# Kernel tuning notes

Hardware: AMD Instinct MI355X
Metric: run time of the kernel (lower is better)

The kernel has to match this reference:

```python
import jax, jax.numpy as jnp
import numpy as np

HEADS = 8
CONTEXT_FRAMES = 128
REL_POS_MAX = 128


def setup_inputs() -> dict:
    key = jax.random.key(0)
    ks = jax.random.split(key, 6)
    b, c, f, t = 2, 512, 64, 512
    x = jax.random.normal(ks[0], (b, c, f, t), dtype=jnp.float32)
    # Linear weights stored as [in, out] (equivalent to torch weight.T)
    W_qkv = jax.random.normal(ks[1], (c, 3 * c), dtype=jnp.float32) * (c ** -0.5)
    b_qkv = jnp.zeros((3 * c,), dtype=jnp.float32)
    W_proj = jax.random.normal(ks[2], (c, c), dtype=jnp.float32) * (c ** -0.5)
    b_proj = jnp.zeros((c,), dtype=jnp.float32)
    rel_pos_bias = jax.random.normal(ks[3], (HEADS, REL_POS_MAX), dtype=jnp.float32) * 0.02
    return {"x": x, "W_qkv": W_qkv, "b_qkv": b_qkv, "W_proj": W_proj,
            "b_proj": b_proj, "rel_pos_bias": rel_pos_bias}


def reference(x, W_qkv, b_qkv, W_proj, b_proj, rel_pos_bias):
    b, c, f, t = x.shape
    hd = c // HEADS
    # (b, c, f, t) -> (b*f, t, c)
    h = jnp.transpose(x, (0, 2, 3, 1)).reshape(b * f, t, c)
    qkv = (h @ W_qkv + b_qkv).reshape(b * f, t, 3, HEADS, hd)
    q, k, v = qkv[:, :, 0], qkv[:, :, 1], qkv[:, :, 2]  # [bf, t, H, hd]
    scale = hd ** -0.5
    scores = jnp.einsum('nqhd,nkhd->nhqk', q, k) * scale  # [bf, H, t, t]
    # causal band mask + gathered relative-position bias
    dist = jnp.arange(t)[:, None] - jnp.arange(t)[None, :]  # [t, t]
    invalid = (dist < 0) | (dist >= CONTEXT_FRAMES)
    bias = rel_pos_bias[:, jnp.clip(dist, 0, REL_POS_MAX - 1)]  # [H, t, t]
    scores = scores + bias[None]
    scores = jnp.where(invalid[None, None], -jnp.inf, scores)
    attn = jax.nn.softmax(scores, axis=-1)
    y = jnp.einsum('nhqk,nkhd->nqhd', attn, v).reshape(b * f, t, c)
    y = y @ W_proj + b_proj
    return jnp.transpose(y.reshape(b, f, t, c), (0, 3, 1, 2))
```

## Files before the change

kernel.cpp:

```cpp
#include <hip/hip_runtime.h>
#include <hip/hip_bf16.h>

typedef short s16x8 __attribute__((ext_vector_type(8)));
typedef unsigned short u16x4 __attribute__((ext_vector_type(4)));
typedef float f32x4 __attribute__((ext_vector_type(4)));

#define MFMA16(a,b,c) __builtin_amdgcn_mfma_f32_16x16x32_bf16((a),(b),(c),0,0,0)

__device__ __forceinline__ unsigned short f2bf(float x){
  unsigned int u = __float_as_uint(x);
  u += 0x7fffu + ((u >> 16) & 1u);
  return (unsigned short)(u >> 16);
}

__device__ __forceinline__ void gl_lds16(const unsigned short* g, unsigned short* l){
  __builtin_amdgcn_global_load_lds((const __attribute__((address_space(1))) unsigned int*)g,
                                   (__attribute__((address_space(3))) unsigned int*)l, 16, 0, 0);
}

__global__ void __launch_bounds__(256) wt_prep(const float* __restrict__ Wq, const float* __restrict__ Wp,
                                               unsigned short* __restrict__ WqT, unsigned short* __restrict__ WpT){
  __shared__ unsigned short tb[64][65];
  int blk = blockIdx.x;
  const float* src; unsigned short* dst; int N, k0, n0;
  if (blk < 192){
    src = Wq; dst = WqT; N = 1536;
    n0 = (blk % 24)*64; k0 = (blk / 24)*64;
  } else {
    blk -= 192; src = Wp; dst = WpT; N = 512;
    n0 = (blk & 7)*64; k0 = (blk >> 3)*64;
  }
  const int tid = threadIdx.x;
  const int nl = tid & 63;
  #pragma unroll
  for (int it = 0; it < 16; ++it){
    const int kl = it*4 + (tid >> 6);
    tb[kl][nl] = f2bf(src[(size_t)(k0+kl)*N + n0 + nl]);
  }
  __syncthreads();
  const int c2 = (tid & 31)*2;
  #pragma unroll
  for (int it = 0; it < 8; ++it){
    const int nw = it*8 + (tid >> 5);
    unsigned int v = (unsigned int)tb[c2][nw] | ((unsigned int)tb[c2+1][nw] << 16);
    *(unsigned int*)(dst + (size_t)(n0+nw)*512 + k0 + c2) = v;
  }
}

__global__ void __launch_bounds__(256) x_to_h(const float* __restrict__ x, unsigned short* __restrict__ h){
  __shared__ unsigned short tb[64][65];
  const int blk = blockIdx.x;
  const int ttt = blk & 7, cht = (blk >> 3) & 7, n = blk >> 6;
  const int b = n >> 6, f = n & 63;
  const int t = threadIdx.x;
  const int tt0 = ttt*64, ch0 = cht*64;
  const float* xb = x + ((size_t)(b*512 + ch0)*64 + f)*512 + tt0;
  const int ttl = t & 63;
  #pragma unroll
  for (int it = 0; it < 16; ++it){
    const int chl = it*4 + (t >> 6);
    tb[chl][ttl] = f2bf(xb[(size_t)chl*32768 + ttl]);
  }
  __syncthreads();
  unsigned short* hb = h + ((size_t)n*512 + tt0)*512 + ch0;
  const int c2 = (t & 31)*2;
  #pragma unroll
  for (int it = 0; it < 8; ++it){
    const int ttw = it*8 + (t >> 5);
    unsigned int v = (unsigned int)tb[c2][ttw] | ((unsigned int)tb[c2+1][ttw] << 16);
    *(unsigned int*)(hb + (size_t)ttw*512 + c2) = v;
  }
}

__device__ __forceinline__ void gemm_core_256(const unsigned short* __restrict__ A,
                                              const unsigned short* __restrict__ Bt,
                                              char* smem, int bm, int bn, int tid,
                                              f32x4 (&acc)[8][4]){
  const int lane = tid & 63, w = tid >> 6;
  const int wm = w >> 2, wn = w & 3;
  const int lq = lane & 15, lg = lane >> 4;
  const unsigned short* Ag[4]; const unsigned short* Bg[4]; int wub[4];
  #pragma unroll
  for (int j = 0; j < 4; ++j){
    const int slot = j*512 + tid;
    const int srow = slot >> 3;
    const int sg = (slot & 7) ^ (srow & 7);
    Ag[j] = A  + (size_t)(bm*256 + srow)*512 + sg*8;
    Bg[j] = Bt + (size_t)(bn*256 + srow)*512 + sg*8;
    wub[j] = (j*512 + w*64)*8;
  }
  unsigned short* LA[2] = {(unsigned short*)smem,           (unsigned short*)(smem + 65536)};
  unsigned short* LB[2] = {(unsigned short*)(smem + 32768), (unsigned short*)(smem + 98304)};
  int raby[8], rbby[4];
  #pragma unroll
  for (int i = 0; i < 8; ++i) raby[i] = (wm*128 + i*16 + lq)*128;
  #pragma unroll
  for (int j = 0; j < 4; ++j) rbby[j] = (wn*64 + j*16 + lq)*128;
  const int cg0 = ((lg    ) ^ (lq & 7))*16;
  const int cg1 = ((4 + lg) ^ (lq & 7))*16;
  #pragma unroll
  for (int j = 0; j < 4; ++j){ gl_lds16(Ag[j], LA[0] + wub[j]); gl_lds16(Bg[j], LB[0] + wub[j]); }
  __syncthreads();
  for (int kt = 0; kt < 8; ++kt){
    const int cur = kt & 1;
    const char* Ab = (const char*)LA[cur];
    const char* Bb = (const char*)LB[cur];
    unsigned short* An = LA[cur^1]; unsigned short* Bn = LB[cur^1];
    const int nko = (kt + 1)*64;
    const bool st = (kt < 7);
    s16x8 a[4][2], b0[2][2], b1[2][2];
    #pragma unroll
    for (int i = 0; i < 4; ++i){
      a[i][0] = *(const s16x8*)(Ab + raby[i] + cg0);
      a[i][1] = *(const s16x8*)(Ab + raby[i] + cg1);
    }
    #pragma unroll
    for (int j = 0; j < 2; ++j){
      b0[j][0] = *(const s16x8*)(Bb + rbby[j] + cg0);
      b0[j][1] = *(const s16x8*)(Bb + rbby[j] + cg1);
    }
    if (st){ gl_lds16(Ag[0] + nko, An + wub[0]); gl_lds16(Ag[1] + nko, An + wub[1]); }
    __builtin_amdgcn_sched_barrier(0);
    __builtin_amdgcn_s_barrier();
    __builtin_amdgcn_sched_barrier(0);
    __builtin_amdgcn_s_setprio(1);
    #pragma unroll
    for (int i = 0; i < 4; ++i)
      #pragma unroll
      for (int j = 0; j < 2; ++j){
        acc[i][j] = MFMA16(a[i][0], b0[j][0], acc[i][j]);
        acc[i][j] = MFMA16(a[i][1], b0[j][1], acc[i][j]);
      }
    __builtin_amdgcn_s_setprio(0);
    __builtin_amdgcn_sched_barrier(0);
    __builtin_amdgcn_s_barrier();
    __builtin_amdgcn_sched_barrier(0);
    #pragma unroll
    for (int j = 0; j < 2; ++j){
      b1[j][0] = *(const s16x8*)(Bb + rbby[2+j] + cg0);
      b1[j][1] = *(const s16x8*)(Bb + rbby[2+j] + cg1);
    }
    if (st){ gl_lds16(Ag[2] + nko, An + wub[2]); gl_lds16(Ag[3] + nko, An + wub[3]); }
    __builtin_amdgcn_sched_barrier(0);
    __builtin_amdgcn_s_barrier();
    __builtin_amdgcn_sched_barrier(0);
    __builtin_amdgcn_s_setprio(1);
    #pragma unroll
    for (int i = 0; i < 4; ++i)
      #pragma unroll
      for (int j = 0; j < 2; ++j){
        acc[i][2+j] = MFMA16(a[i][0], b1[j][0], acc[i][2+j]);
        acc[i][2+j] = MFMA16(a[i][1], b1[j][1], acc[i][2+j]);
      }
    __builtin_amdgcn_s_setprio(0);
    __builtin_amdgcn_sched_barrier(0);
    __builtin_amdgcn_s_barrier();
    __builtin_amdgcn_sched_barrier(0);
    #pragma unroll
    for (int i = 0; i < 4; ++i){
      a[i][0] = *(const s16x8*)(Ab + raby[4+i] + cg0);
      a[i][1] = *(const s16x8*)(Ab + raby[4+i] + cg1);
    }
    if (st){ gl_lds16(Bg[0] + nko, Bn + wub[0]); gl_lds16(Bg[1] + nko, Bn + wub[1]); }
    __builtin_amdgcn_sched_barrier(0);
    __builtin_amdgcn_s_barrier();
    __builtin_amdgcn_sched_barrier(0);
    __builtin_amdgcn_s_setprio(1);
    #pragma unroll
    for (int i = 0; i < 4; ++i)
      #pragma unroll
      for (int j = 0; j < 2; ++j){
        acc[4+i][j] = MFMA16(a[i][0], b0[j][0], acc[4+i][j]);
        acc[4+i][j] = MFMA16(a[i][1], b0[j][1], acc[4+i][j]);
      }
    __builtin_amdgcn_s_setprio(0);
    __builtin_amdgcn_sched_barrier(0);
    __builtin_amdgcn_s_barrier();
    __builtin_amdgcn_sched_barrier(0);
    if (st){ gl_lds16(Bg[2] + nko, Bn + wub[2]); gl_lds16(Bg[3] + nko, Bn + wub[3]); }
    __builtin_amdgcn_sched_barrier(0);
    __builtin_amdgcn_s_barrier();
    __builtin_amdgcn_sched_barrier(0);
    __builtin_amdgcn_s_setprio(1);
    #pragma unroll
    for (int i = 0; i < 4; ++i)
      #pragma unroll
      for (int j = 0; j < 2; ++j){
        acc[4+i][2+j] = MFMA16(a[i][0], b1[j][0], acc[4+i][2+j]);
        acc[4+i][2+j] = MFMA16(a[i][1], b1[j][1], acc[4+i][2+j]);
      }
    __builtin_amdgcn_s_setprio(0);
    __syncthreads();
  }
}

__global__ void __launch_bounds__(512, 2) qkv_gemm256(const unsigned short* __restrict__ h,
                                                      const unsigned short* __restrict__ WqT,
                                                      const float* __restrict__ bqkv,
                                                      unsigned short* __restrict__ Qb,
                                                      unsigned short* __restrict__ Kb,
                                                      unsigned short* __restrict__ Vt){
  extern __shared__ __align__(16) char smem[];
  const int tid = threadIdx.x;
  const int orig = blockIdx.x;
  const int wg = (orig & 7)*192 + (orig >> 3);
  const int bm = wg / 6, bn = wg % 6;
  f32x4 acc[8][4] = {};
  gemm_core_256(h, WqT, smem, bm, bn, tid, acc);
  const int lane = tid & 63, w = tid >> 6;
  const int wm = w >> 2, wn = w & 3;
  const int lq = lane & 15, lg = lane >> 4;
  float bj[4];
  #pragma unroll
  for (int j = 0; j < 4; ++j) bj[j] = bqkv[bn*256 + wn*64 + j*16 + lq];
  const int n = bm >> 1, tt0 = (bm & 1)*256;
  const int sel = bn >> 1, cq0 = (bn & 1)*256;
  unsigned short* Cs = (unsigned short*)smem;
  #pragma unroll
  for (int mh = 0; mh < 2; ++mh){
    __syncthreads();
    if (wm == mh){
      #pragma unroll
      for (int i = 0; i < 8; ++i)
        #pragma unroll
        for (int j = 0; j < 4; ++j)
          #pragma unroll
          for (int r = 0; r < 4; ++r)
            Cs[(i*16 + lg*4 + r)*264 + wn*64 + j*16 + lq] = f2bf(acc[i][j][r] + bj[j]);
    }
    __syncthreads();
    if (sel < 2){
      unsigned short* dst = (sel == 0) ? Qb : Kb;
      #pragma unroll
      for (int it = 0; it < 8; ++it){
        const int idx = it*512 + tid;
        const int rowl = idx >> 5, c8 = (idx & 31)*8;
        const int cq = cq0 + c8, head = cq >> 6, d0 = cq & 63;
        const int tg = tt0 + mh*128 + rowl;
        *(s16x8*)(dst + ((size_t)(n*8 + head)*512 + tg)*64 + d0) = *(const s16x8*)(Cs + rowl*264 + c8);
      }
    } else {
      const int col = tid >> 1;
      const int cq = cq0 + col, head = cq >> 6, d = cq & 63;
      #pragma unroll
      for (int seg = 0; seg < 8; ++seg){
        const int r0 = (tid & 1)*64 + seg*8;
        s16x8 v;
        #pragma unroll
        for (int r = 0; r < 8; ++r) v[r] = (short)Cs[(r0 + r)*264 + col];
        const int tg0 = tt0 + mh*128 + r0;
        *(s16x8*)(Vt + ((size_t)(n*8 + head)*64 + d)*512 + tg0) = v;
      }
    }
  }
}

__global__ void __launch_bounds__(512, 2) proj_gemm256(const unsigned short* __restrict__ ys,
                                                       const unsigned short* __restrict__ WpT,
                                                       const float* __restrict__ bproj,
                                                       float* __restrict__ out){
  extern __shared__ __align__(16) char smem[];
  const int tid = threadIdx.x;
  const int orig = blockIdx.x;
  const int wg = (orig & 7)*64 + (orig >> 3);
  const int bm = wg >> 1, bn = wg & 1;
  f32x4 acc[8][4] = {};
  gemm_core_256(ys, WpT, smem, bm, bn, tid, acc);
  const int lane = tid & 63, w = tid >> 6;
  const int wm = w >> 2, wn = w & 3;
  const int lq = lane & 15, lg = lane >> 4;
  float bj[4];
  #pragma unroll
  for (int j = 0; j < 4; ++j) bj[j] = bproj[bn*256 + wn*64 + j*16 + lq];
  const int n = bm >> 1, tt0 = (bm & 1)*256;
  const int b = n >> 6, f = n & 63;
  float* Csf = (float*)smem;
  #pragma unroll
  for (int mh = 0; mh < 2; ++mh){
    __syncthreads();
    if (wm == mh){
      #pragma unroll
      for (int i = 0; i < 8; ++i)
        #pragma unroll
        for (int j = 0; j < 4; ++j)
          #pragma unroll
          for (int r = 0; r < 4; ++r)
            Csf[(i*16 + lg*4 + r)*256 + wn*64 + j*16 + lq] = acc[i][j][r] + bj[j];
    }
    __syncthreads();
    const int ch = tid >> 1;
    const int chg = bn*256 + ch;
    #pragma unroll
    for (int s = 0; s < 16; ++s){
      const int r0 = (tid & 1)*64 + s*4;
      f32x4 v;
      #pragma unroll
      for (int r = 0; r < 4; ++r) v[r] = Csf[(r0 + r)*256 + ch];
      const int tg = tt0 + mh*128 + r0;
      *(f32x4*)(out + ((size_t)(b*512 + chg)*64 + f)*512 + tg) = v;
    }
  }
}

__global__ void __launch_bounds__(256) attn_kernel(const unsigned short* __restrict__ Qb,
                                                   const unsigned short* __restrict__ Kb,
                                                   const unsigned short* __restrict__ Vt,
                                                   const float* __restrict__ relb,
                                                   unsigned short* __restrict__ ys){
  __shared__ __align__(16) unsigned short KsL[2][4096];
  __shared__ __align__(16) unsigned short VsL[2][4096];
  __shared__ __align__(16) unsigned short P[4][2][16*72];
  __shared__ float biasS[128];
  const int blk = blockIdx.x;
  const int qt = blk & 3, hh = (blk >> 2) & 7, n = blk >> 5;
  const int tid = threadIdx.x, lane = tid & 63, w = tid >> 6;
  if (tid < 128) biasS[tid] = relb[hh*128 + tid];
  const int q0 = qt * 128;
  const size_t nh = (size_t)(n*8 + hh);
  const unsigned short* Kbase = Kb + nh*32768;
  const unsigned short* Vbase = Vt + nh*32768;
  const int lq = lane & 15, lg = lane >> 4;
  const int qq0 = q0 + w*32;
  s16x8 bq[2][2];
  #pragma unroll
  for (int qs = 0; qs < 2; ++qs){
    const unsigned short* Qp = Qb + (nh*512 + qq0 + qs*16 + lq)*64 + lg*8;
    bq[qs][0] = *(const s16x8*)(Qp);
    bq[qs][1] = *(const s16x8*)(Qp + 32);
  }
  int r_[2], g_[2], dsl_[2];
  #pragma unroll
  for (int j = 0; j < 2; ++j){
    const int slot = j*256 + w*64 + lane;
    r_[j] = slot >> 3;
    g_[j] = (slot & 7) ^ (r_[j] & 7);
    dsl_[j] = (j*256 + w*64) * 8;
  }
  f32x4 yacc[2][4] = {{{0.f,0.f,0.f,0.f}}};
  float m_run[2] = {-INFINITY, -INFINITY}, l_run[2] = {0.f, 0.f};
  const int first = (q0 >= 128) ? 0 : ((128 - q0 + 63) >> 6);
  int cur = 0;
  {
    const int kt0 = q0 - 128 + first*64;
    #pragma unroll
    for (int j = 0; j < 2; ++j){
      gl_lds16(Kbase + (size_t)(kt0 + r_[j])*64 + g_[j]*8, KsL[0] + dsl_[j]);
      gl_lds16(Vbase + (size_t)r_[j]*512 + kt0 + g_[j]*8,  VsL[0] + dsl_[j]);
    }
  }
  for (int kt = first; kt < 4; ++kt){
    const int kt0 = q0 - 128 + kt*64;
    __syncthreads();
    if (kt < 3){
      const int nk0 = kt0 + 64;
      #pragma unroll
      for (int j = 0; j < 2; ++j){
        gl_lds16(Kbase + (size_t)(nk0 + r_[j])*64 + g_[j]*8, KsL[cur^1] + dsl_[j]);
        gl_lds16(Vbase + (size_t)r_[j]*512 + nk0 + g_[j]*8,  VsL[cur^1] + dsl_[j]);
      }
    }
    const bool wact = (kt0 <= qq0 + 31);
    if (wact){
      s16x8 av[4][2];
      #pragma unroll
      for (int mk = 0; mk < 4; ++mk){
        const int rr = mk*16 + lq;
        const unsigned short* kp = KsL[cur] + rr*64;
        av[mk][0] = *(const s16x8*)(kp + ((lg     ) ^ (rr & 7))*8);
        av[mk][1] = *(const s16x8*)(kp + ((4 + lg ) ^ (rr & 7))*8);
      }
      float pex[2][4][4];
      #pragma unroll
      for (int qs = 0; qs < 2; ++qs){
        const int qqs = qq0 + qs*16;
        if (kt0 > qqs + 15 || kt0 + 63 < qqs - 127) continue;
        f32x4 s4[4] = {{0.f,0.f,0.f,0.f}};
        #pragma unroll
        for (int mk = 0; mk < 4; ++mk){
          s4[mk] = MFMA16(av[mk][0], bq[qs][0], s4[mk]);
          s4[mk] = MFMA16(av[mk][1], bq[qs][1], s4[mk]);
        }
        const int qg = qqs + lq;
        float pmax = -3.0e38f;
        #pragma unroll
        for (int mk = 0; mk < 4; ++mk)
          #pragma unroll
          for (int r = 0; r < 4; ++r){
            const int dist = qg - (kt0 + mk*16 + lg*4 + r);
            float xv;
            if (dist >= 0 && dist < 128) xv = s4[mk][r]*0.125f + biasS[dist];
            else                         xv = -1.0e30f;
            pex[qs][mk][r] = xv;
            pmax = fmaxf(pmax, xv);
          }
        pmax = fmaxf(pmax, __shfl_xor(pmax, 16, 64));
        pmax = fmaxf(pmax, __shfl_xor(pmax, 32, 64));
        const float m_new = fmaxf(m_run[qs], pmax);
        const float scalef = __expf(m_run[qs] - m_new);
        float psum = 0.f;
        unsigned short* Pw = P[w][qs];
        #pragma unroll
        for (int mk = 0; mk < 4; ++mk){
          u16x4 pk;
          #pragma unroll
          for (int r = 0; r < 4; ++r){
            const float pe = __expf(pex[qs][mk][r] - m_new);
            psum += pe;
            pk[r] = f2bf(pe);
          }
          *(u16x4*)(Pw + lq*72 + mk*16 + lg*4) = pk;
        }
        psum += __shfl_xor(psum, 16, 64);
        psum += __shfl_xor(psum, 32, 64);
        l_run[qs] = l_run[qs]*scalef + psum;
        m_run[qs] = m_new;
        #pragma unroll
        for (int i = 0; i < 4; ++i) yacc[qs][i] *= scalef;
      }
      s16x8 vv[4][2];
      #pragma unroll
      for (int i = 0; i < 4; ++i){
        const int rr = i*16 + lq;
        const unsigned short* vp = VsL[cur] + rr*64;
        vv[i][0] = *(const s16x8*)(vp + ((lg    ) ^ (rr & 7))*8);
        vv[i][1] = *(const s16x8*)(vp + ((4 + lg) ^ (rr & 7))*8);
      }
      #pragma unroll
      for (int qs = 0; qs < 2; ++qs){
        const int qqs = qq0 + qs*16;
        if (kt0 > qqs + 15 || kt0 + 63 < qqs - 127) continue;
        unsigned short* Pw = P[w][qs];
        #pragma unroll
        for (int ks2 = 0; ks2 < 2; ++ks2){
          s16x8 pb = *(const s16x8*)(Pw + lq*72 + ks2*32 + lg*8);
          #pragma unroll
          for (int i = 0; i < 4; ++i)
            yacc[qs][i] = MFMA16(vv[i][ks2], pb, yacc[qs][i]);
        }
      }
    }
    cur ^= 1;
  }
  #pragma unroll
  for (int qs = 0; qs < 2; ++qs){
    const float inv = 1.f / l_run[qs];
    unsigned short* yp = ys + ((size_t)n*512 + qq0 + qs*16 + lq)*512 + hh*64 + lg*4;
    #pragma unroll
    for (int i = 0; i < 4; ++i){
      u16x4 o;
      #pragma unroll
      for (int r = 0; r < 4; ++r) o[r] = f2bf(yacc[qs][i][r]*inv);
      *(u16x4*)(yp + i*16) = o;
    }
  }
}

extern "C" void kernel_launch(void* const* d_in, const int* in_sizes, int n_in,
                              void* d_out, int out_size, void* d_ws, size_t ws_size,
                              hipStream_t stream){
  const float* x     = (const float*)d_in[0];
  const float* Wqkv  = (const float*)d_in[1];
  const float* bqkv  = (const float*)d_in[2];
  const float* Wproj = (const float*)d_in[3];
  const float* bproj = (const float*)d_in[4];
  const float* relb  = (const float*)d_in[5];
  float* out = (float*)d_out;
  char* ws = (char*)d_ws;
  if (ws_size < (size_t)270532608) return;
  unsigned short* hbuf = (unsigned short*)(ws);
  unsigned short* Qb   = (unsigned short*)(ws + (size_t)67108864);
  unsigned short* Kb   = (unsigned short*)(ws + (size_t)134217728);
  unsigned short* Vt   = (unsigned short*)(ws + (size_t)201326592);
  unsigned short* WqT  = (unsigned short*)(ws + (size_t)268435456);
  unsigned short* WpT  = (unsigned short*)(ws + (size_t)270008320);

  hipFuncSetAttribute(reinterpret_cast<const void*>(qkv_gemm256),
                      hipFuncAttributeMaxDynamicSharedMemorySize, 131072);
  hipFuncSetAttribute(reinterpret_cast<const void*>(proj_gemm256),
                      hipFuncAttributeMaxDynamicSharedMemorySize, 131072);

  hipLaunchKernelGGL(wt_prep,      dim3(256),  dim3(256), 0, stream, Wqkv, Wproj, WqT, WpT);
  hipLaunchKernelGGL(x_to_h,       dim3(8192), dim3(256), 0, stream, x, hbuf);
  hipLaunchKernelGGL(qkv_gemm256,  dim3(1536), dim3(512), 131072, stream, hbuf, WqT, bqkv, Qb, Kb, Vt);
  hipLaunchKernelGGL(attn_kernel,  dim3(4096), dim3(256), 0, stream, Qb, Kb, Vt, relb, hbuf);
  hipLaunchKernelGGL(proj_gemm256, dim3(512),  dim3(512), 131072, stream, hbuf, WpT, bproj, out);
}
```

Baseline: 395.1 us.

## Restructure GEMM core into 4-stage K=32 LDS pipeline with vmcnt-based waits

Replaces the two-buffer, K=64 main loop of the shared 256x256 GEMM core with a four-buffer pipeline over sixteen K=32 steps. Loads are issued three steps ahead, and completion is tracked with explicit s_waitcnt vmcnt values plus a single barrier per step, instead of several barriers per K tile. The LDS layout and swizzle change to pack two rows per 128-byte line for the narrower K slice. The aim is to hide global-to-LDS latency and cut barrier overhead. The cost is hand-tuned wait counts that must match the issue pattern exactly, and the same 128 KB of LDS.

```diff
diff --git a/kernel.cpp b/kernel.cpp
--- a/kernel.cpp
+++ b/kernel.cpp
@@ -79,119 +79,61 @@
   const int lane = tid & 63, w = tid >> 6;
   const int wm = w >> 2, wn = w & 3;
   const int lq = lane & 15, lg = lane >> 4;
-  const unsigned short* Ag[4]; const unsigned short* Bg[4]; int wub[4];
-  #pragma unroll
-  for (int j = 0; j < 4; ++j){
-    const int slot = j*512 + tid;
-    const int srow = slot >> 3;
-    const int sg = (slot & 7) ^ (srow & 7);
-    Ag[j] = A  + (size_t)(bm*256 + srow)*512 + sg*8;
-    Bg[j] = Bt + (size_t)(bn*256 + srow)*512 + sg*8;
+  const unsigned short* Agp[2]; const unsigned short* Bgp[2]; int wub[2];
+  #pragma unroll
+  for (int j = 0; j < 2; ++j){
+    const int u = j*512 + tid;
+    const int p = u >> 3, Gs = u & 7;
+    const int G = Gs ^ (p & 7);
+    const int row = p*2 + (G >> 2), g = G & 3;
+    Agp[j] = A  + (size_t)(bm*256 + row)*512 + g*8;
+    Bgp[j] = Bt + (size_t)(bn*256 + row)*512 + g*8;
     wub[j] = (j*512 + w*64)*8;
   }
-  unsigned short* LA[2] = {(unsigned short*)smem,           (unsigned short*)(smem + 65536)};
-  unsigned short* LB[2] = {(unsigned short*)(smem + 32768), (unsigned short*)(smem + 98304)};
-  int raby[8], rbby[4];
-  #pragma unroll
-  for (int i = 0; i < 8; ++i) raby[i] = (wm*128 + i*16 + lq)*128;
-  #pragma unroll
-  for (int j = 0; j < 4; ++j) rbby[j] = (wn*64 + j*16 + lq)*128;
-  const int cg0 = ((lg    ) ^ (lq & 7))*16;
-  const int cg1 = ((4 + lg) ^ (lq & 7))*16;
-  #pragma unroll
-  for (int j = 0; j < 4; ++j){ gl_lds16(Ag[j], LA[0] + wub[j]); gl_lds16(Bg[j], LB[0] + wub[j]); }
-  __syncthreads();
-  for (int kt = 0; kt < 8; ++kt){
-    const int cur = kt & 1;
-    const char* Ab = (const char*)LA[cur];
-    const char* Bb = (const char*)LB[cur];
-    unsigned short* An = LA[cur^1]; unsigned short* Bn = LB[cur^1];
-    const int nko = (kt + 1)*64;
-    const bool st = (kt < 7);
-    s16x8 a[4][2], b0[2][2], b1[2][2];
-    #pragma unroll
-    for (int i = 0; i < 4; ++i){
-      a[i][0] = *(const s16x8*)(Ab + raby[i] + cg0);
-      a[i][1] = *(const s16x8*)(Ab + raby[i] + cg1);
-    }
-    #pragma unroll
-    for (int j = 0; j < 2; ++j){
-      b0[j][0] = *(const s16x8*)(Bb + rbby[j] + cg0);
-      b0[j][1] = *(const s16x8*)(Bb + rbby[j] + cg1);
-    }
-    if (st){ gl_lds16(Ag[0] + nko, An + wub[0]); gl_lds16(Ag[1] + nko, An + wub[1]); }
-    __builtin_amdgcn_sched_barrier(0);
-    __builtin_amdgcn_s_barrier();
-    __builtin_amdgcn_sched_barrier(0);
-    __builtin_amdgcn_s_setprio(1);
-    #pragma unroll
-    for (int i = 0; i < 4; ++i)
-      #pragma unroll
-      for (int j = 0; j < 2; ++j){
-        acc[i][j] = MFMA16(a[i][0], b0[j][0], acc[i][j]);
-        acc[i][j] = MFMA16(a[i][1], b0[j][1], acc[i][j]);
-      }
-    __builtin_amdgcn_s_setprio(0);
-    __builtin_amdgcn_sched_barrier(0);
-    __builtin_amdgcn_s_barrier();
-    __builtin_amdgcn_sched_barrier(0);
-    #pragma unroll
-    for (int j = 0; j < 2; ++j){
-      b1[j][0] = *(const s16x8*)(Bb + rbby[2+j] + cg0);
-      b1[j][1] = *(const s16x8*)(Bb + rbby[2+j] + cg1);
-    }
-    if (st){ gl_lds16(Ag[2] + nko, An + wub[2]); gl_lds16(Ag[3] + nko, An + wub[3]); }
-    __builtin_amdgcn_sched_barrier(0);
-    __builtin_amdgcn_s_barrier();
-    __builtin_amdgcn_sched_barrier(0);
-    __builtin_amdgcn_s_setprio(1);
-    #pragma unroll
-    for (int i = 0; i < 4; ++i)
-      #pragma unroll
-      for (int j = 0; j < 2; ++j){
-        acc[i][2+j] = MFMA16(a[i][0], b1[j][0], acc[i][2+j]);
-        acc[i][2+j] = MFMA16(a[i][1], b1[j][1], acc[i][2+j]);
-      }
-    __builtin_amdgcn_s_setprio(0);
-    __builtin_amdgcn_sched_barrier(0);
-    __builtin_amdgcn_s_barrier();
-    __builtin_amdgcn_sched_barrier(0);
-    #pragma unroll
-    for (int i = 0; i < 4; ++i){
-      a[i][0] = *(const s16x8*)(Ab + raby[4+i] + cg0);
-      a[i][1] = *(const s16x8*)(Ab + raby[4+i] + cg1);
-    }
-    if (st){ gl_lds16(Bg[0] + nko, Bn + wub[0]); gl_lds16(Bg[1] + nko, Bn + wub[1]); }
-    __builtin_amdgcn_sched_barrier(0);
-    __builtin_amdgcn_s_barrier();
-    __builtin_amdgcn_sched_barrier(0);
-    __builtin_amdgcn_s_setprio(1);
-    #pragma unroll
-    for (int i = 0; i < 4; ++i)
-      #pragma unroll
-      for (int j = 0; j < 2; ++j){
-        acc[4+i][j] = MFMA16(a[i][0], b0[j][0], acc[4+i][j]);
-        acc[4+i][j] = MFMA16(a[i][1], b0[j][1], acc[4+i][j]);
-      }
-    __builtin_amdgcn_s_setprio(0);
-    __builtin_amdgcn_sched_barrier(0);
-    __builtin_amdgcn_s_barrier();
-    __builtin_amdgcn_sched_barrier(0);
-    if (st){ gl_lds16(Bg[2] + nko, Bn + wub[2]); gl_lds16(Bg[3] + nko, Bn + wub[3]); }
-    __builtin_amdgcn_sched_barrier(0);
-    __builtin_amdgcn_s_barrier();
-    __builtin_amdgcn_sched_barrier(0);
-    __builtin_amdgcn_s_setprio(1);
-    #pragma unroll
-    for (int i = 0; i < 4; ++i)
-      #pragma unroll
-      for (int j = 0; j < 2; ++j){
-        acc[4+i][2+j] = MFMA16(a[i][0], b1[j][0], acc[4+i][2+j]);
-        acc[4+i][2+j] = MFMA16(a[i][1], b1[j][1], acc[4+i][2+j]);
-      }
-    __builtin_amdgcn_s_setprio(0);
-    __syncthreads();
-  }
+  unsigned short* Lbase = (unsigned short*)smem;
+  const int lqh = lq >> 1;
+  const int gx16 = (((lq & 1)*4 + lg) ^ lqh) * 16;
+  const int wmA = wm*64;
+  const int wnB = wn*32;
+
+#define GST_ISSUE(SK) { \
+    unsigned short* An_ = Lbase + ((SK)&3)*16384; \
+    const int ko_ = (SK)*32; \
+    gl_lds16(Agp[0] + ko_, An_ + wub[0]); \
+    gl_lds16(Agp[1] + ko_, An_ + wub[1]); \
+    gl_lds16(Bgp[0] + ko_, An_ + 8192 + wub[0]); \
+    gl_lds16(Bgp[1] + ko_, An_ + 8192 + wub[1]); }
+
+#define GSTEP(S, VM) { \
+    if ((S) + 3 < 16) GST_ISSUE((S)+3); \
+    const char* Ab_ = (const char*)(Lbase + ((S)&3)*16384); \
+    const char* Bb_ = Ab_ + 16384; \
+    s16x8 a_[8], b_[4]; \
+    _Pragma("unroll") for (int i = 0; i < 8; ++i) \
+      a_[i] = *(const s16x8*)(Ab_ + (wmA + i*8 + lqh)*128 + gx16); \
+    _Pragma("unroll") for (int j = 0; j < 4; ++j) \
+      b_[j] = *(const s16x8*)(Bb_ + (wnB + j*8 + lqh)*128 + gx16); \
+    __builtin_amdgcn_s_setprio(1); \
+    _Pragma("unroll") for (int i = 0; i < 8; ++i) \
+      _Pragma("unroll") for (int j = 0; j < 4; ++j) \
+        acc[i][j] = MFMA16(a_[i], b_[j], acc[i][j]); \
+    __builtin_amdgcn_s_setprio(0); \
+    asm volatile("s_waitcnt vmcnt(" VM ")" ::: "memory"); \
+    __builtin_amdgcn_sched_barrier(0); \
+    __builtin_amdgcn_s_barrier(); \
+    __builtin_amdgcn_sched_barrier(0); }
+
+  GST_ISSUE(0); GST_ISSUE(1); GST_ISSUE(2);
+  asm volatile("s_waitcnt vmcnt(8)" ::: "memory");
+  __builtin_amdgcn_sched_barrier(0);
+  __builtin_amdgcn_s_barrier();
+  __builtin_amdgcn_sched_barrier(0);
+  GSTEP(0,"8");  GSTEP(1,"8");  GSTEP(2,"8");  GSTEP(3,"8");
+  GSTEP(4,"8");  GSTEP(5,"8");  GSTEP(6,"8");  GSTEP(7,"8");
+  GSTEP(8,"8");  GSTEP(9,"8");  GSTEP(10,"8"); GSTEP(11,"8");
+  GSTEP(12,"8"); GSTEP(13,"4"); GSTEP(14,"0"); GSTEP(15,"0");
+#undef GSTEP
+#undef GST_ISSUE
 }
 
 __global__ void __launch_bounds__(512, 2) qkv_gemm256(const unsigned short* __restrict__ h,
```

New measurement: 393.4 us. No clear change (-0.4%).
